# Kernel optimization log

Measured on AMD Instinct MI355X. Metric: run time of the kernel, lower is better.

Reference implementation:

```python
import jax, jax.numpy as jnp
import numpy as np

HIDDEN = 1024
INTER = 4096

def setup_inputs() -> dict:
    key = jax.random.key(0)
    k1, k2, k3, k4, k5 = jax.random.split(key, 5)
    hidden_states = jax.random.normal(k1, (4, 2048, HIDDEN), dtype=jnp.float32)
    # Linear params: W stored pre-transposed as [in, out], matching W = dense.weight.t()
    W1 = jax.random.normal(k2, (HIDDEN, INTER), dtype=jnp.float32) * (1.0 / np.sqrt(HIDDEN))
    b1 = jax.random.normal(k3, (INTER,), dtype=jnp.float32) * 0.02
    W2 = jax.random.normal(k4, (INTER, HIDDEN), dtype=jnp.float32) * (1.0 / np.sqrt(INTER))
    b2 = jax.random.normal(k5, (HIDDEN,), dtype=jnp.float32) * 0.02
    return {"hidden_states": hidden_states, "W1": W1, "b1": b1, "W2": W2, "b2": b2}

def reference(hidden_states, W1, b1, W2, b2):
    # Tiled loops in the original are exactly a dense 2-layer MLP with ReLU.
    h = jax.nn.relu(jnp.einsum('bsh,hi->bsi', hidden_states, W1) + b1)
    return jnp.einsum('bsi,ih->bsh', h, W2) + b2
```

## Files before the change

kernel.cpp:

```cpp
#include <hip/hip_runtime.h>
#include <cstddef>

typedef short short8 __attribute__((ext_vector_type(8)));
typedef unsigned short ushort8 __attribute__((ext_vector_type(8)));
typedef float f32x4 __attribute__((ext_vector_type(4)));

#define AS1(p) ((const __attribute__((address_space(1))) void*)(p))
#define AS3(p) ((__attribute__((address_space(3))) void*)(p))

__device__ __forceinline__ unsigned short f2bf(float f) {
  unsigned int u = __builtin_bit_cast(unsigned int, f);
  u += 0x7FFFu + ((u >> 16) & 1u);
  return (unsigned short)(u >> 16);
}

__device__ __forceinline__ void gload_lds16(const void* g, void* l) {
  __builtin_amdgcn_global_load_lds(AS1(g), AS3(l), 16, 0, 0);
}

template <int N>
__device__ __forceinline__ void vwait() {
  asm volatile("s_waitcnt vmcnt(%0)" :: "n"(N) : "memory");
}

__global__ __launch_bounds__(256)
void prep_fused(const float* __restrict__ X,
                const float* __restrict__ W1,
                const float* __restrict__ W2,
                unsigned short* __restrict__ Xbf,
                unsigned short* __restrict__ W1t,
                unsigned short* __restrict__ W2t) {
  const int b   = blockIdx.x;
  const int tid = threadIdx.x;

  if (b >= 8192) {
    const size_t i = (size_t)(b - 8192) * 256 + tid;
    float4 v = *reinterpret_cast<const float4*>(X + i * 4);
    ushort4 o;
    o.x = f2bf(v.x); o.y = f2bf(v.y); o.z = f2bf(v.z); o.w = f2bf(v.w);
    *reinterpret_cast<ushort4*>(Xbf + i * 4) = o;
    return;
  }

  __shared__ float tile[32][33];
  const float* in;
  unsigned short* out;
  int Kd, Nd, n0, k0;
  if (b < 4096) {
    in = W1; out = W1t; Kd = 1024; Nd = 4096;
    n0 = (b & 127) * 32;
    k0 = (b >> 7) * 32;
  } else {
    const int b2 = b - 4096;
    in = W2; out = W2t; Kd = 4096; Nd = 1024;
    n0 = (b2 & 31) * 32;
    k0 = (b2 >> 5) * 32;
  }
  const int tx = tid & 31;
  const int ty = tid >> 5;
#pragma unroll
  for (int i = 0; i < 4; ++i)
    tile[ty + i * 8][tx] = in[(size_t)(k0 + ty + i * 8) * Nd + n0 + tx];
  __syncthreads();
#pragma unroll
  for (int i = 0; i < 4; ++i)
    out[(size_t)(n0 + ty + i * 8) * Kd + k0 + tx] = f2bf(tile[tx][ty + i * 8]);
}

__global__ void cvt_f32_bf16(const float* __restrict__ in,
                             unsigned short* __restrict__ out, int n4) {
  int i = blockIdx.x * blockDim.x + threadIdx.x;
  if (i >= n4) return;
  float4 v = *reinterpret_cast<const float4*>(in + (size_t)i * 4);
  ushort4 o;
  o.x = f2bf(v.x); o.y = f2bf(v.y); o.z = f2bf(v.z); o.w = f2bf(v.w);
  *reinterpret_cast<ushort4*>(out + (size_t)i * 4) = o;
}

__global__ void transpose_cvt(const float* __restrict__ in,
                              unsigned short* __restrict__ out,
                              int Kd, int Nd) {
  __shared__ float tile[32][33];
  const int n0 = blockIdx.x * 32;
  const int k0 = blockIdx.y * 32;
  const int tx = threadIdx.x;
  const int ty = threadIdx.y;
#pragma unroll
  for (int i = 0; i < 4; ++i)
    tile[ty + i * 8][tx] = in[(size_t)(k0 + ty + i * 8) * Nd + n0 + tx];
  __syncthreads();
#pragma unroll
  for (int i = 0; i < 4; ++i)
    out[(size_t)(n0 + ty + i * 8) * Kd + k0 + tx] = f2bf(tile[tx][ty + i * 8]);
}

#define QPH(D, QM, QN, RDA, RDB, STAGE, WAITC)                                 \
  {                                                                            \
    if (RDA) {                                                                 \
      char* ab = lds + (D) * 32768 + (QM) * 16384;                             \
      _Pragma("unroll")                                                        \
      for (int mi = 0; mi < 4; ++mi)                                           \
        _Pragma("unroll")                                                      \
        for (int kk = 0; kk < 2; ++kk)                                         \
          aF[mi][kk] = *reinterpret_cast<const short8*>(ab + ardA[mi][kk]);    \
    }                                                                          \
    if (RDB) {                                                                 \
      char* bb = lds + 65536 + (D) * 2 * BHB + (QN) * BHB;                     \
      _Pragma("unroll")                                                        \
      for (int ni = 0; ni < NF; ++ni)                                          \
        _Pragma("unroll")                                                      \
        for (int kk = 0; kk < 2; ++kk)                                         \
          bF[QN][ni][kk] = *reinterpret_cast<const short8*>(bb + brdB[ni][kk]);\
    }                                                                          \
    STAGE;                                                                     \
    __builtin_amdgcn_s_setprio(1);                                             \
    _Pragma("unroll")                                                          \
    for (int mi = 0; mi < 4; ++mi)                                             \
      _Pragma("unroll")                                                        \
      for (int ni = 0; ni < NF; ++ni)                                          \
        _Pragma("unroll")                                                      \
        for (int kk = 0; kk < 2; ++kk)                                         \
          acc[QM][QN][mi][ni] = __builtin_amdgcn_mfma_f32_16x16x32_bf16(       \
              aF[mi][kk], bF[QN][ni][kk], acc[QM][QN][mi][ni], 0, 0, 0);       \
    __builtin_amdgcn_s_setprio(0);                                             \
    WAITC;                                                                     \
    __builtin_amdgcn_s_barrier();                                              \
  }

template <int BN, int RELU_BF16_OUT>
__global__ __launch_bounds__(512, 2)
void gemm_q(const unsigned short* __restrict__ A, int lda,
            const unsigned short* __restrict__ B, int ldb,
            const float* __restrict__ bias,
            void* __restrict__ C, int ldc, int K, int nbx) {
  constexpr int NF  = BN / 128;
  constexpr int LA  = 2;
  constexpr int LB  = BN / 128;
  constexpr int BHB = BN * 64;
  extern __shared__ char lds[];

  const int tid  = threadIdx.x;
  const int lane = tid & 63;
  const int wid  = tid >> 6;
  const int wm2  = wid >> 2;
  const int wn4  = wid & 3;

  const int cpx     = gridDim.x >> 3;
  const int logical = (blockIdx.x & 7) * cpx + (blockIdx.x >> 3);
  const int m0 = (logical / nbx) * 256;
  const int n0 = (logical % nbx) * BN;

  f32x4 acc[2][2][4][NF];
#pragma unroll
  for (int a = 0; a < 2; ++a)
#pragma unroll
    for (int b = 0; b < 2; ++b)
#pragma unroll
      for (int c = 0; c < 4; ++c)
#pragma unroll
        for (int d = 0; d < NF; ++d)
          acc[a][b][c][d] = (f32x4){0.f, 0.f, 0.f, 0.f};

  size_t aG[2], bG[2];
#pragma unroll
  for (int u = 0; u < 2; ++u) {
    const int s   = (u * 512 + tid) * 16;
    const int nat = s ^ (((s >> 7) & 7) << 4);
    aG[u] = (size_t)(m0 + (nat >> 7)) * lda + ((nat & 127) >> 1);
    if (u < LB)
      bG[u] = (size_t)(n0 + (nat >> 7)) * ldb + ((nat & 127) >> 1);
    else
      bG[u] = 0;
  }
  const int wb0 = (tid & 448) * 16;
  const int wb1 = 8192 + wb0;

  auto stageA = [&](int d, int h, int kel) {
    char* dst = lds + d * 32768 + h * 16384;
    gload_lds16(A + aG[0] + (size_t)h * 128 * lda + kel, dst + wb0);
    gload_lds16(A + aG[1] + (size_t)h * 128 * lda + kel, dst + wb1);
  };
  auto stageB = [&](int d, int h, int kel) {
    char* dst = lds + 65536 + d * 2 * BHB + h * BHB;
    gload_lds16(B + bG[0] + (size_t)h * (BN / 2) * ldb + kel, dst + wb0);
    if constexpr (LB == 2)
      gload_lds16(B + bG[1] + (size_t)h * (BN / 2) * ldb + kel, dst + wb1);
  };

  int ardA[4][2], brdB[NF][2];
#pragma unroll
  for (int mi = 0; mi < 4; ++mi)
#pragma unroll
    for (int kk = 0; kk < 2; ++kk) {
      const int nat = (wm2 * 64 + mi * 16 + (lane & 15)) * 128 +
                      kk * 64 + (lane >> 4) * 16;
      ardA[mi][kk] = nat ^ (((nat >> 7) & 7) << 4);
    }
#pragma unroll
  for (int ni = 0; ni < NF; ++ni)
#pragma unroll
    for (int kk = 0; kk < 2; ++kk) {
      const int nat = (wn4 * (BN / 8) + ni * 16 + (lane & 15)) * 128 +
                      kk * 64 + (lane >> 4) * 16;
      brdB[ni][kk] = nat ^ (((nat >> 7) & 7) << 4);
    }

  stageA(0, 0, 0);
  stageB(0, 0, 0);
  stageB(0, 1, 0);
  stageA(0, 1, 0);
  vwait<LA + LB>();
  __builtin_amdgcn_s_barrier();

  short8 aF[4][2];
  short8 bF[2][NF][2];
  const int NT = K >> 6;
  for (int it = 0; it < NT - 1; ++it) {
    const int d = it & 1, e = d ^ 1;
    const int nk = (it + 1) << 6;
    QPH(d, 0, 0, 1, 1, stageA(e, 0, nk), vwait<2 * LA>());
    QPH(d, 0, 1, 0, 1, stageB(e, 0, nk), (vwait<LA + LB>()));
    QPH(d, 1, 0, 1, 0, stageB(e, 1, nk), vwait<2 * LB>());
    QPH(d, 1, 1, 0, 0, stageA(e, 1, nk), (vwait<LB + LA>()));
  }
  {
    const int d = (NT - 1) & 1;
    QPH(d, 0, 0, 1, 1, ((void)0), vwait<LA>());
    QPH(d, 0, 1, 0, 1, ((void)0), vwait<0>());
    QPH(d, 1, 0, 1, 0, ((void)0), ((void)0));
    QPH(d, 1, 1, 0, 0, ((void)0), ((void)0));
  }

  __syncthreads();
  {
#pragma unroll
    for (int qm = 0; qm < 2; ++qm) {
#pragma unroll
      for (int qn = 0; qn < 2; ++qn) {
#pragma unroll
        for (int ni = 0; ni < NF; ++ni) {
          const int c = qn * (BN / 2) + wn4 * (BN / 8) + ni * 16 + (lane & 15);
          const float bv = bias[n0 + c];
#pragma unroll
          for (int mi = 0; mi < 4; ++mi) {
#pragma unroll
            for (int rr = 0; rr < 4; ++rr) {
              const int row = qm * 128 + wm2 * 64 + mi * 16 +
                              (lane >> 4) * 4 + rr;
              float v = acc[qm][qn][mi][ni][rr] + bv;
              if (RELU_BF16_OUT) {
                v = v > 0.f ? v : 0.f;
                const int byte = (row * 512 + c * 2) ^ ((row & 7) << 4);
                *reinterpret_cast<unsigned short*>(lds + byte) = f2bf(v);
              } else {
                const int byte = (row * 512 + c * 4) ^ ((row & 7) << 4);
                *reinterpret_cast<float*>(lds + byte) = v;
              }
            }
          }
        }
      }
    }
    __syncthreads();
#pragma unroll
    for (int i = 0; i < 16; ++i) {
      const int idx  = i * 512 + tid;
      const int row  = idx >> 5;
      const int g    = idx & 31;
      const int byte = (row * 512 + g * 16) ^ ((row & 7) << 4);
      const uint4 val = *reinterpret_cast<const uint4*>(lds + byte);
      if (RELU_BF16_OUT) {
        unsigned short* dst = (unsigned short*)C +
            (size_t)(m0 + row) * ldc + n0 + g * 8;
        *reinterpret_cast<uint4*>(dst) = val;
      } else {
        float* dst = (float*)C + (size_t)(m0 + row) * ldc + n0 + g * 4;
        *reinterpret_cast<uint4*>(dst) = val;
      }
    }
  }
}

template <int A_F32, int RELU_BF16_OUT>
__global__ __launch_bounds__(256, 2)
void gemm_bf16(const void* __restrict__ Ap, int lda,
               const unsigned short* __restrict__ B, int ldb,
               const float* __restrict__ bias,
               void* __restrict__ C, int ldc,
               int K, int beta) {
  __shared__ char lds[32768];
  char* const As = lds;
  char* const Bs = lds + 16384;

  const int tid  = threadIdx.x;
  const int lane = tid & 63;
  const int w    = tid >> 6;
  const int wm   = w >> 1;
  const int wn   = w & 1;
  const int m0   = blockIdx.y * 128;
  const int n0   = blockIdx.x * 128;

  f32x4 acc[4][4];
#pragma unroll
  for (int i = 0; i < 4; ++i)
#pragma unroll
    for (int j = 0; j < 4; ++j)
      acc[i][j] = (f32x4){0.f, 0.f, 0.f, 0.f};

  int srow[4], scol[4], sbase[4];
#pragma unroll
  for (int j = 0; j < 4; ++j) {
    const int stored  = (j * 256 + tid) * 16;
    const int natural = stored ^ (((stored >> 7) & 7) << 4);
    srow[j]  = natural >> 7;
    scol[j]  = (natural & 127) >> 1;
    sbase[j] = (j * 256 + (tid & 192)) * 16;
  }

  size_t agofs[4];
  int ast[4];
  if (A_F32) {
#pragma unroll
    for (int pq = 0; pq < 4; ++pq) {
      const int idx = pq * 256 + tid;
      const int rr  = idx >> 3;
      const int kbe = (idx & 7) * 8;
      agofs[pq] = (size_t)(m0 + rr) * lda + kbe;
      const int nat = rr * 128 + kbe * 2;
      ast[pq] = nat ^ (((nat >> 7) & 7) << 4);
    }
  }

  const int nsteps = K >> 6;
  for (int ks = 0; ks < nsteps; ++ks) {
    const int k0 = ks << 6;
    if (A_F32) {
      const float* Af = (const float*)Ap;
#pragma unroll
      for (int pq = 0; pq < 4; ++pq) {
        const float* sp = Af + agofs[pq] + k0;
        float4 x0 = *reinterpret_cast<const float4*>(sp);
        float4 x1 = *reinterpret_cast<const float4*>(sp + 4);
        ushort8 v;
        v[0] = f2bf(x0.x); v[1] = f2bf(x0.y); v[2] = f2bf(x0.z); v[3] = f2bf(x0.w);
        v[4] = f2bf(x1.x); v[5] = f2bf(x1.y); v[6] = f2bf(x1.z); v[7] = f2bf(x1.w);
        *reinterpret_cast<ushort8*>(As + ast[pq]) = v;
      }
    } else {
      const unsigned short* Ab = (const unsigned short*)Ap;
#pragma unroll
      for (int j = 0; j < 4; ++j)
        gload_lds16(Ab + (size_t)(m0 + srow[j]) * lda + (k0 + scol[j]),
                    As + sbase[j]);
    }
#pragma unroll
    for (int j = 0; j < 4; ++j)
      gload_lds16(B + (size_t)(n0 + srow[j]) * ldb + (k0 + scol[j]),
                  Bs + sbase[j]);
    __syncthreads();

#pragma unroll
    for (int kk = 0; kk < 2; ++kk) {
      const int kb = kk * 64 + (lane >> 4) * 16;
      short8 af[4], bfv[4];
#pragma unroll
      for (int mi = 0; mi < 4; ++mi) {
        int nat = (wm * 64 + mi * 16 + (lane & 15)) * 128 + kb;
        int st  = nat ^ (((nat >> 7) & 7) << 4);
        af[mi] = *reinterpret_cast<const short8*>(As + st);
      }
#pragma unroll
      for (int ni = 0; ni < 4; ++ni) {
        int nat = (wn * 64 + ni * 16 + (lane & 15)) * 128 + kb;
        int st  = nat ^ (((nat >> 7) & 7) << 4);
        bfv[ni] = *reinterpret_cast<const short8*>(Bs + st);
      }
#pragma unroll
      for (int mi = 0; mi < 4; ++mi)
#pragma unroll
        for (int ni = 0; ni < 4; ++ni)
          acc[mi][ni] = __builtin_amdgcn_mfma_f32_16x16x32_bf16(
              af[mi], bfv[ni], acc[mi][ni], 0, 0, 0);
    }
    __syncthreads();
  }

  const int row0 = m0 + wm * 64 + (lane >> 4) * 4;
  const int col0 = n0 + wn * 64 + (lane & 15);
#pragma unroll
  for (int ni = 0; ni < 4; ++ni) {
    const int c = col0 + ni * 16;
    const float bv = beta ? 0.f : bias[c];
#pragma unroll
    for (int mi = 0; mi < 4; ++mi) {
#pragma unroll
      for (int rr = 0; rr < 4; ++rr) {
        const size_t idx = (size_t)(row0 + mi * 16 + rr) * ldc + c;
        float v = acc[mi][ni][rr] + bv;
        if (RELU_BF16_OUT) {
          v = v > 0.f ? v : 0.f;
          ((unsigned short*)C)[idx] = f2bf(v);
        } else {
          if (beta) v += ((float*)C)[idx];
          ((float*)C)[idx] = v;
        }
      }
    }
  }
}

extern "C" void kernel_launch(void* const* d_in, const int* in_sizes, int n_in,
                              void* d_out, int out_size, void* d_ws, size_t ws_size,
                              hipStream_t stream) {
  const float* X  = (const float*)d_in[0];
  const float* W1 = (const float*)d_in[1];
  const float* b1 = (const float*)d_in[2];
  const float* W2 = (const float*)d_in[3];
  const float* b2 = (const float*)d_in[4];
  float* out = (float*)d_out;

  const int M = 8192, H = 1024, I = 4096;
  const size_t MB = 1024 * 1024;

  char* ws = (char*)d_ws;
  unsigned short* W1t = (unsigned short*)ws;
  unsigned short* W2t = (unsigned short*)(ws + 8 * MB);

  if (ws_size >= 80 * MB) {
    unsigned short* Xbf = (unsigned short*)((char*)d_out + 16 * MB);
    unsigned short* Hbf = (unsigned short*)(ws + 16 * MB);
    prep_fused<<<16384, 256, 0, stream>>>(X, W1, W2, Xbf, W1t, W2t);
    gemm_q<256, 1><<<512, 512, 131072, stream>>>(
        Xbf, H, W1t, H, b1, Hbf, I, H, I / 256);
    gemm_q<128, 0><<<256, 512, 131072, stream>>>(
        Hbf, I, W2t, I, b2, out, H, I, H / 128);
    return;
  }

  transpose_cvt<<<dim3(I / 32, H / 32), dim3(32, 8), 0, stream>>>(W1, W1t, H, I);
  transpose_cvt<<<dim3(H / 32, I / 32), dim3(32, 8), 0, stream>>>(W2, W2t, I, H);

  int Ic, useXbf;
  unsigned short* Xbf = nullptr;
  unsigned short* Hc;
  if (ws_size >= 64 * MB) {
    Ic = 2048; useXbf = 1;
    Xbf = (unsigned short*)(ws + 16 * MB);
    Hc  = (unsigned short*)(ws + 32 * MB);
  } else if (ws_size >= 48 * MB) {
    Ic = 1024; useXbf = 1;
    Xbf = (unsigned short*)(ws + 16 * MB);
    Hc  = (unsigned short*)(ws + 32 * MB);
  } else if (ws_size >= 32 * MB) {
    Ic = 1024; useXbf = 0;
    Hc  = (unsigned short*)(ws + 16 * MB);
  } else if (ws_size >= 24 * MB) {
    Ic = 512;  useXbf = 0;
    Hc  = (unsigned short*)(ws + 16 * MB);
  } else if (ws_size >= 20 * MB) {
    Ic = 256;  useXbf = 0;
    Hc  = (unsigned short*)(ws + 16 * MB);
  } else {
    Ic = 128;  useXbf = 0;
    Hc  = (unsigned short*)(ws + 16 * MB);
  }

  if (useXbf) {
    int n4 = (M * H) / 4;
    cvt_f32_bf16<<<(n4 + 255) / 256, 256, 0, stream>>>(X, Xbf, n4);
  }

  const int nch = I / Ic;
  for (int c = 0; c < nch; ++c) {
    const int i0 = c * Ic;
    if (useXbf)
      gemm_bf16<0, 1><<<dim3(Ic / 128, M / 128), 256, 0, stream>>>(
          Xbf, H, W1t + (size_t)i0 * H, H, b1 + i0, Hc, Ic, H, 0);
    else
      gemm_bf16<1, 1><<<dim3(Ic / 128, M / 128), 256, 0, stream>>>(
          X, H, W1t + (size_t)i0 * H, H, b1 + i0, Hc, Ic, H, 0);
    gemm_bf16<0, 0><<<dim3(H / 128, M / 128), 256, 0, stream>>>(
        Hc, Ic, W2t + i0, I, b2, out, H, Ic, c > 0);
  }
}
```

Baseline: 157.2 us.

## Prefetch next quadrant's LDS fragments during MFMA phase with double-buffered A registers

```diff
diff --git a/kernel.cpp b/kernel.cpp
--- a/kernel.cpp
+++ b/kernel.cpp
@@ -94,25 +94,10 @@
     out[(size_t)(n0 + ty + i * 8) * Kd + k0 + tx] = f2bf(tile[tx][ty + i * 8]);
 }
 
-#define QPH(D, QM, QN, RDA, RDB, STAGE, WAITC)                                 \
+#define QP3(QM, QN, AF, RDNEXT, STAGE, WAITC)                                  \
   {                                                                            \
-    if (RDA) {                                                                 \
-      char* ab = lds + (D) * 32768 + (QM) * 16384;                             \
-      _Pragma("unroll")                                                        \
-      for (int mi = 0; mi < 4; ++mi)                                           \
-        _Pragma("unroll")                                                      \
-        for (int kk = 0; kk < 2; ++kk)                                         \
-          aF[mi][kk] = *reinterpret_cast<const short8*>(ab + ardA[mi][kk]);    \
-    }                                                                          \
-    if (RDB) {                                                                 \
-      char* bb = lds + 65536 + (D) * 2 * BHB + (QN) * BHB;                     \
-      _Pragma("unroll")                                                        \
-      for (int ni = 0; ni < NF; ++ni)                                          \
-        _Pragma("unroll")                                                      \
-        for (int kk = 0; kk < 2; ++kk)                                         \
-          bF[QN][ni][kk] = *reinterpret_cast<const short8*>(bb + brdB[ni][kk]);\
-    }                                                                          \
-    STAGE;                                                                     \
+    asm volatile("s_waitcnt lgkmcnt(0)" ::: "memory");                         \
+    __builtin_amdgcn_sched_barrier(0);                                         \
     __builtin_amdgcn_s_setprio(1);                                             \
     _Pragma("unroll")                                                          \
     for (int mi = 0; mi < 4; ++mi)                                             \
@@ -121,18 +106,21 @@
         _Pragma("unroll")                                                      \
         for (int kk = 0; kk < 2; ++kk)                                         \
           acc[QM][QN][mi][ni] = __builtin_amdgcn_mfma_f32_16x16x32_bf16(       \
-              aF[mi][kk], bF[QN][ni][kk], acc[QM][QN][mi][ni], 0, 0, 0);       \
+              AF[mi][kk], bF[QN][ni][kk], acc[QM][QN][mi][ni], 0, 0, 0);       \
     __builtin_amdgcn_s_setprio(0);                                             \
+    RDNEXT;                                                                    \
+    STAGE;                                                                     \
     WAITC;                                                                     \
+    __builtin_amdgcn_sched_barrier(0);                                         \
     __builtin_amdgcn_s_barrier();                                              \
   }
 
 template <int BN, int RELU_BF16_OUT>
 __global__ __launch_bounds__(512, 2)
-void gemm_q(const unsigned short* __restrict__ A, int lda,
-            const unsigned short* __restrict__ B, int ldb,
-            const float* __restrict__ bias,
-            void* __restrict__ C, int ldc, int K, int nbx) {
+void gemm_q3(const unsigned short* __restrict__ A, int lda,
+             const unsigned short* __restrict__ B, int ldb,
+             const float* __restrict__ bias,
+             void* __restrict__ C, int ldc, int K, int nbx) {
   constexpr int NF  = BN / 128;
   constexpr int LA  = 2;
   constexpr int LB  = BN / 128;
@@ -205,30 +193,63 @@
       brdB[ni][kk] = nat ^ (((nat >> 7) & 7) << 4);
     }
 
+  short8 aF0[4][2], aF1[4][2];
+  short8 bF[2][NF][2];
+
+  auto rdB1 = [&](int dd) {
+    char* bb = lds + 65536 + dd * 2 * BHB + BHB;
+#pragma unroll
+    for (int ni = 0; ni < NF; ++ni)
+#pragma unroll
+      for (int kk = 0; kk < 2; ++kk)
+        bF[1][ni][kk] = *reinterpret_cast<const short8*>(bb + brdB[ni][kk]);
+  };
+  auto rdA1 = [&](int dd) {
+    char* ab = lds + dd * 32768 + 16384;
+#pragma unroll
+    for (int mi = 0; mi < 4; ++mi)
+#pragma unroll
+      for (int kk = 0; kk < 2; ++kk)
+        aF1[mi][kk] = *reinterpret_cast<const short8*>(ab + ardA[mi][kk]);
+  };
+  auto rdAB0 = [&](int ee) {
+    char* ab = lds + ee * 32768;
+#pragma unroll
+    for (int mi = 0; mi < 4; ++mi)
+#pragma unroll
+      for (int kk = 0; kk < 2; ++kk)
+        aF0[mi][kk] = *reinterpret_cast<const short8*>(ab + ardA[mi][kk]);
+    char* bb = lds + 65536 + ee * 2 * BHB;
+#pragma unroll
+    for (int ni = 0; ni < NF; ++ni)
+#pragma unroll
+      for (int kk = 0; kk < 2; ++kk)
+        bF[0][ni][kk] = *reinterpret_cast<const short8*>(bb + brdB[ni][kk]);
+  };
+
   stageA(0, 0, 0);
   stageB(0, 0, 0);
   stageB(0, 1, 0);
   stageA(0, 1, 0);
-  vwait<LA + LB>();
+  vwait<LA>();
   __builtin_amdgcn_s_barrier();
-
-  short8 aF[4][2];
-  short8 bF[2][NF][2];
+  rdAB0(0);
+
   const int NT = K >> 6;
   for (int it = 0; it < NT - 1; ++it) {
     const int d = it & 1, e = d ^ 1;
     const int nk = (it + 1) << 6;
-    QPH(d, 0, 0, 1, 1, stageA(e, 0, nk), vwait<2 * LA>());
-    QPH(d, 0, 1, 0, 1, stageB(e, 0, nk), (vwait<LA + LB>()));
-    QPH(d, 1, 0, 1, 0, stageB(e, 1, nk), vwait<2 * LB>());
-    QPH(d, 1, 1, 0, 0, stageA(e, 1, nk), (vwait<LB + LA>()));
+    QP3(0, 0, aF0, rdB1(d),   stageA(e, 0, nk), vwait<LA>());
+    QP3(0, 1, aF0, rdA1(d),   stageB(e, 0, nk), ((void)0));
+    QP3(1, 0, aF1, ((void)0), stageB(e, 1, nk), vwait<LB>());
+    QP3(1, 1, aF1, rdAB0(e),  stageA(e, 1, nk), vwait<LA>());
   }
   {
     const int d = (NT - 1) & 1;
-    QPH(d, 0, 0, 1, 1, ((void)0), vwait<LA>());
-    QPH(d, 0, 1, 0, 1, ((void)0), vwait<0>());
-    QPH(d, 1, 0, 1, 0, ((void)0), ((void)0));
-    QPH(d, 1, 1, 0, 0, ((void)0), ((void)0));
+    QP3(0, 0, aF0, rdB1(d),   ((void)0), vwait<0>());
+    QP3(0, 1, aF0, rdA1(d),   ((void)0), ((void)0));
+    QP3(1, 0, aF1, ((void)0), ((void)0), ((void)0));
+    QP3(1, 1, aF1, ((void)0), ((void)0), ((void)0));
   }
 
   __syncthreads();
@@ -430,9 +451,9 @@
     unsigned short* Xbf = (unsigned short*)((char*)d_out + 16 * MB);
     unsigned short* Hbf = (unsigned short*)(ws + 16 * MB);
     prep_fused<<<16384, 256, 0, stream>>>(X, W1, W2, Xbf, W1t, W2t);
-    gemm_q<256, 1><<<512, 512, 131072, stream>>>(
+    gemm_q3<256, 1><<<512, 512, 131072, stream>>>(
         Xbf, H, W1t, H, b1, Hbf, I, H, I / 256);
-    gemm_q<128, 0><<<256, 512, 131072, stream>>>(
+    gemm_q3<128, 0><<<256, 512, 131072, stream>>>(
         Hbf, I, W2t, I, b2, out, H, I, H / 128);
     return;
   }
```

Result: slower. 164.1 us (+4.4%).
